# Optimization experiments

Hardware: AMD Instinct MI355X
Metric: run time of the kernel (lower is better)

## Reference

```python
import jax, jax.numpy as jnp
import numpy as np

# ---- config (mirrors init_kwargs) ----
T = 1024          # num tokens (one causal sequence)
H = 1024          # hidden_size
NQ, NK, D = 16, 4, 64   # q heads, kv heads, head_dim (GQA)
I_DENSE = 4096    # dense FFN intermediate
I_MOE = 512       # expert FFN intermediate
E, K = 8, 2       # num_experts, top_k
EPS = 1e-6
THETA = 10000.0


def setup_inputs() -> dict:
    key = jax.random.key(0)
    ks = jax.random.split(key, 20)
    rn = lambda k, shp: (jax.random.normal(k, shp, dtype=jnp.float32) * 0.02)
    QKV = (NQ + 2 * NK) * D
    return {
        "hidden_states": jax.random.normal(ks[0], (T, H), dtype=jnp.float32),
        "residual": jax.random.normal(ks[1], (T, H), dtype=jnp.float32),
        "positions": jnp.arange(T, dtype=jnp.int32),
        "ln0_w": jnp.ones((H,), jnp.float32),
        "pa0_w": jnp.ones((H,), jnp.float32),
        "ln1_w": jnp.ones((H,), jnp.float32),
        "pa1_w": jnp.ones((H,), jnp.float32),
        # attention weights (stored [in, out] so x @ W)
        "qkv0_w": rn(ks[2], (H, QKV)),
        "o0_w": rn(ks[3], (NQ * D, H)),
        "qkv1_w": rn(ks[4], (H, QKV)),
        "o1_w": rn(ks[5], (NQ * D, H)),
        # dense MLPs (merged gate_up: first half gate, second half up)
        "gu0_w": rn(ks[6], (H, 2 * I_DENSE)),
        "dn0_w": rn(ks[7], (I_DENSE, H)),
        "gu1_w": rn(ks[8], (H, 2 * I_DENSE)),
        "dn1_w": rn(ks[9], (I_DENSE, H)),
        # MoE: router gate + per-expert SwiGLU weights
        "gate_w": rn(ks[10], (H, E)),
        "w13": rn(ks[11], (E, H, 2 * I_MOE)),
        "w2": rn(ks[12], (E, I_MOE, H)),
    }


def _rmsnorm(x, w):
    v = jnp.mean(jnp.square(x.astype(jnp.float32)), axis=-1, keepdims=True)
    return (x.astype(jnp.float32) * jax.lax.rsqrt(v + EPS)).astype(x.dtype) * w


def _add_rmsnorm(x, res, w):
    # sglang fused add + RMSNorm: residual <- x + residual; out <- rmsnorm(residual)
    res = x + res
    return _rmsnorm(res, w), res


def _rope(pos, x):
    # neox-style rotary over full head_dim; x: [T, n_heads, D]
    half = D // 2
    inv_freq = 1.0 / (THETA ** (jnp.arange(half, dtype=jnp.float32) / half))
    f = pos.astype(jnp.float32)[:, None] * inv_freq            # [T, half]
    cos, sin = jnp.cos(f)[:, None, :], jnp.sin(f)[:, None, :]  # [T, 1, half]
    x1, x2 = x[..., :half], x[..., half:]
    return jnp.concatenate([x1 * cos - x2 * sin, x2 * cos + x1 * sin], axis=-1)


def _attention(pos, x, qkv_w, o_w):
    qkv = x @ qkv_w
    q = qkv[:, : NQ * D].reshape(T, NQ, D)
    k = qkv[:, NQ * D : (NQ + NK) * D].reshape(T, NK, D)
    v = qkv[:, (NQ + NK) * D :].reshape(T, NK, D)
    q, k = _rope(pos, q), _rope(pos, k)
    g = NQ // NK
    qg = q.reshape(T, NK, g, D)
    scores = jnp.einsum("tkgd,skd->kgts", qg, k) * (D ** -0.5)  # [NK,g,T,T]
    causal = jnp.tril(jnp.ones((T, T), bool))
    scores = jnp.where(causal, scores, jnp.float32(-1e30))
    p = jax.nn.softmax(scores, axis=-1)
    o = jnp.einsum("kgts,skd->tkgd", p, v).reshape(T, NQ * D)
    return o @ o_w


def _dense_mlp(x, gu_w, dn_w):
    gu = x @ gu_w
    h = jax.nn.silu(gu[:, :I_DENSE]) * gu[:, I_DENSE:]  # SiluAndMul
    return h @ dn_w


def _moe(x, gate_w, w13, w2):
    # router in fp32 (router_dtype == 'float32'), softmax, top-k, no renormalize
    logits = x.astype(jnp.float32) @ gate_w.astype(jnp.float32)  # [T, E]
    probs = jax.nn.softmax(logits, axis=-1)
    topw, topi = jax.lax.top_k(probs, K)                         # [T, K]
    rows = jnp.arange(x.shape[0])[:, None]
    combine = jnp.zeros((x.shape[0], E), jnp.float32).at[rows, topi].set(topw)
    combine = combine.astype(x.dtype)
    out = jnp.zeros_like(x)
    for e in range(E):  # fixed small expert count: grouped-GEMM reference
        g = x @ w13[e]
        h = jax.nn.silu(g[:, :I_MOE]) * g[:, I_MOE:]
        out = out + combine[:, e : e + 1] * (h @ w2[e])
    return out


def reference(hidden_states, residual, positions, ln0_w, pa0_w, ln1_w, pa1_w,
              qkv0_w, o0_w, qkv1_w, o1_w, gu0_w, dn0_w, gu1_w, dn1_w,
              gate_w, w13, w2):
    h, r = _add_rmsnorm(hidden_states, residual, ln0_w)
    h = _attention(positions, h, qkv0_w, o0_w)
    h, r = _add_rmsnorm(h, r, pa0_w)
    shortcut = _moe(h, gate_w, w13, w2)      # MoE runs on the shortcut branch
    h = _dense_mlp(h, gu0_w, dn0_w)
    h, r = _add_rmsnorm(h, r, ln1_w)
    h = _attention(positions, h, qkv1_w, o1_w)
    h, r = _add_rmsnorm(h, r, pa1_w)
    h = _dense_mlp(h, gu1_w, dn1_w)
    h = h + shortcut                          # combine shortcut MoE output
    return h, r
```

## Files before the change

### kernel.cpp

```cpp
#include <hip/hip_runtime.h>
#include <math.h>

namespace {

constexpr int kT = 1024;
constexpr int kH = 1024;
constexpr int kNQ = 16;
constexpr int kNKV = 4;
constexpr int kD = 64;
constexpr int kQKV = (kNQ + 2 * kNKV) * kD;
constexpr int kIDense = 4096;
constexpr int kIMoe = 512;
constexpr int kE = 8;
constexpr float kEps = 1e-6f;

typedef __attribute__((ext_vector_type(8))) short short8;
typedef __attribute__((ext_vector_type(4))) float f32x4;

__device__ __forceinline__ ushort f2bf(float f) {
    union { float f; uint32_t u; } v; v.f = f;
    uint32_t r = (v.u + 0x7fffu + ((v.u >> 16) & 1u)) >> 16;
    return (ushort)r;
}
__device__ __forceinline__ void gload16(const void* g, void* l) {
    __builtin_amdgcn_global_load_lds(
        (const __attribute__((address_space(1))) void*)g,
        (__attribute__((address_space(3))) void*)l, 16, 0, 0);
}

__global__ __launch_bounds__(256) void add_rmsnorm_kernel(
    const float* __restrict__ x, const float* __restrict__ res,
    const float* __restrict__ w, float* __restrict__ h32,
    ushort* __restrict__ h16, float* __restrict__ r_out)
{
    __shared__ float red[4];
    const int t = blockIdx.x;
    const int i = threadIdx.x;
    const size_t base = (size_t)t * kH;
    float4 a = reinterpret_cast<const float4*>(x + base)[i];
    float4 b = reinterpret_cast<const float4*>(res + base)[i];
    float4 s = make_float4(a.x + b.x, a.y + b.y, a.z + b.z, a.w + b.w);
    reinterpret_cast<float4*>(r_out + base)[i] = s;
    float ss = s.x * s.x + s.y * s.y + s.z * s.z + s.w * s.w;
    #pragma unroll
    for (int off = 32; off > 0; off >>= 1) ss += __shfl_down(ss, off);
    if ((i & 63) == 0) red[i >> 6] = ss;
    __syncthreads();
    const float tot = red[0] + red[1] + red[2] + red[3];
    const float inv = rsqrtf(tot * (1.0f / kH) + kEps);
    float4 wv = reinterpret_cast<const float4*>(w)[i];
    float4 o = make_float4(s.x * inv * wv.x, s.y * inv * wv.y,
                           s.z * inv * wv.z, s.w * inv * wv.w);
    reinterpret_cast<float4*>(h32 + base)[i] = o;
    ushort4 u;
    u.x = f2bf(o.x); u.y = f2bf(o.y); u.z = f2bf(o.z); u.w = f2bf(o.w);
    reinterpret_cast<ushort4*>(h16 + base)[i] = u;
}

__global__ __launch_bounds__(256) void transpose_bf16_kernel(
    const float* __restrict__ W, ushort* __restrict__ WT,
    int R, int Cn, int ld_w, long w_z_stride, long wt_z_stride)
{
    __shared__ float tile[64 * 65];
    const int z = blockIdx.z;
    const float* Wz = W + (size_t)z * w_z_stride;
    ushort* WTz = WT + (size_t)z * wt_z_stride;
    const int r0 = blockIdx.y * 64;
    const int c0 = blockIdx.x * 64;
    const int tid = threadIdx.x;
    const int lr = tid >> 4;
    const int lc = (tid & 15) * 4;
    #pragma unroll
    for (int p = 0; p < 4; p++) {
        const int row = p * 16 + lr;
        float4 v = *reinterpret_cast<const float4*>(
            &Wz[(size_t)(r0 + row) * ld_w + c0 + lc]);
        tile[row * 65 + lc + 0] = v.x;
        tile[row * 65 + lc + 1] = v.y;
        tile[row * 65 + lc + 2] = v.z;
        tile[row * 65 + lc + 3] = v.w;
    }
    __syncthreads();
    const int ocl = tid >> 2;
    const int q = tid & 3;
    ushort u[16];
    #pragma unroll
    for (int e = 0; e < 16; e++)
        u[e] = f2bf(tile[(q * 16 + e) * 65 + ocl]);
    ushort* dst = &WTz[(size_t)(c0 + ocl) * R + r0 + q * 16];
    *reinterpret_cast<short8*>(dst) = *reinterpret_cast<short8*>(&u[0]);
    *reinterpret_cast<short8*>(dst + 8) = *reinterpret_cast<short8*>(&u[8]);
}

template <bool GATED>
__global__ __launch_bounds__(256) void mgemm_kernel(
    const ushort* __restrict__ A, const ushort* __restrict__ B,
    float* __restrict__ Cf, ushort* __restrict__ C16,
    const float* __restrict__ scale,
    int lda, int ldb, int ldc, int kc,
    int gate_off_rows, long b_z_stride, int c_z_col, int k_z_off,
    int scale_stride, int atomic_flag)
{
    __shared__ __align__(16) ushort As[64 * 64];
    __shared__ __align__(16) ushort Bs[64 * 64];
    __shared__ __align__(16) ushort Us[GATED ? 64 * 64 : 8];

    const int z = blockIdx.z;
    const int m0 = blockIdx.y * 64;
    const int n0 = blockIdx.x * 64;
    const int tid = threadIdx.x;
    const ushort* Bz = B + (size_t)z * b_z_stride;
    const int k0 = z * k_z_off;

    const int arow = tid >> 3;
    const int achk = tid & 7;

    const int lane = tid & 63;
    const int wave = tid >> 6;
    const int wr = (wave >> 1) * 32;
    const int wc = (wave & 1) * 32;
    const int lrow = lane & 15;
    const int lg = lane >> 4;

    f32x4 accg[2][2] = {};
    f32x4 accu[2][2] = {};

    for (int kk0 = 0; kk0 < kc; kk0 += 64) {
        const int kbase = k0 + kk0;
        #pragma unroll
        for (int c = 0; c < 2; c++) {
            const int row = c * 32 + arow;
            const int cs = (achk + (row & 7)) & 7;
            gload16(A + (size_t)(m0 + row) * lda + kbase + cs * 8,
                    (char*)As + c * 4096 + tid * 16);
            gload16(Bz + (size_t)(n0 + row) * ldb + kbase + cs * 8,
                    (char*)Bs + c * 4096 + tid * 16);
            if constexpr (GATED)
                gload16(Bz + (size_t)(gate_off_rows + n0 + row) * ldb + kbase + cs * 8,
                        (char*)Us + c * 4096 + tid * 16);
        }
        __syncthreads();

        short8 af[2][2], bfr[2][2];
        #pragma unroll
        for (int mf = 0; mf < 2; mf++)
            #pragma unroll
            for (int kk = 0; kk < 2; kk++) {
                const int r = wr + mf * 16 + lrow;
                const int sl = ((kk * 4 + lg) - (r & 7)) & 7;
                af[mf][kk] = *reinterpret_cast<const short8*>(
                    (const char*)As + r * 128 + sl * 16);
            }
        #pragma unroll
        for (int nf = 0; nf < 2; nf++)
            #pragma unroll
            for (int kk = 0; kk < 2; kk++) {
                const int n = wc + nf * 16 + lrow;
                const int sl = ((kk * 4 + lg) - (n & 7)) & 7;
                bfr[nf][kk] = *reinterpret_cast<const short8*>(
                    (const char*)Bs + n * 128 + sl * 16);
            }
        #pragma unroll
        for (int mf = 0; mf < 2; mf++)
            #pragma unroll
            for (int nf = 0; nf < 2; nf++)
                #pragma unroll
                for (int kk = 0; kk < 2; kk++)
                    accg[mf][nf] = __builtin_amdgcn_mfma_f32_16x16x32_bf16(
                        af[mf][kk], bfr[nf][kk], accg[mf][nf], 0, 0, 0);
        if constexpr (GATED) {
            short8 uf[2][2];
            #pragma unroll
            for (int nf = 0; nf < 2; nf++)
                #pragma unroll
                for (int kk = 0; kk < 2; kk++) {
                    const int n = wc + nf * 16 + lrow;
                    const int sl = ((kk * 4 + lg) - (n & 7)) & 7;
                    uf[nf][kk] = *reinterpret_cast<const short8*>(
                        (const char*)Us + n * 128 + sl * 16);
                }
            #pragma unroll
            for (int mf = 0; mf < 2; mf++)
                #pragma unroll
                for (int nf = 0; nf < 2; nf++)
                    #pragma unroll
                    for (int kk = 0; kk < 2; kk++)
                        accu[mf][nf] = __builtin_amdgcn_mfma_f32_16x16x32_bf16(
                            af[mf][kk], uf[nf][kk], accu[mf][nf], 0, 0, 0);
        }
        __syncthreads();
    }

    const int r4 = (lane >> 4) * 4;
    const int cl = lane & 15;
    const int ccol = z * c_z_col;
    #pragma unroll
    for (int mf = 0; mf < 2; mf++) {
        #pragma unroll
        for (int nf = 0; nf < 2; nf++) {
            #pragma unroll
            for (int j = 0; j < 4; j++) {
                const int row = m0 + wr + mf * 16 + r4 + j;
                const int col = ccol + n0 + wc + nf * 16 + cl;
                if constexpr (GATED) {
                    const float g = accg[mf][nf][j];
                    const float u = accu[mf][nf][j];
                    const float sv =
                        scale ? scale[(size_t)row * scale_stride + z] : 1.0f;
                    const float h = (g / (1.0f + __expf(-g))) * u * sv;
                    C16[(size_t)row * ldc + col] = f2bf(h);
                } else if (atomic_flag) {
                    atomicAdd(&Cf[(size_t)row * ldc + col], accg[mf][nf][j]);
                } else {
                    Cf[(size_t)row * ldc + col] = accg[mf][nf][j];
                }
            }
        }
    }
}

__global__ __launch_bounds__(256) void rope_pack_kernel(
    const float* __restrict__ qkv, const int* __restrict__ positions,
    ushort* __restrict__ Qb, ushort* __restrict__ Kb)
{
    const int t = blockIdx.x;
    const float pos = (float)positions[t];
    for (int item = threadIdx.x; item < (kNQ + kNKV) * 32; item += 256) {
        const int head = item >> 5;
        const int i = item & 31;
        const float inv_freq = powf(10000.0f, -(float)i * (1.0f / 32.0f));
        const float f = pos * inv_freq;
        float sv, cv;
        sincosf(f, &sv, &cv);
        const size_t off = (size_t)t * kQKV + head * kD;
        const float x1 = qkv[off + i];
        const float x2 = qkv[off + 32 + i];
        const float r1 = x1 * cv - x2 * sv;
        const float r2 = x2 * cv + x1 * sv;
        if (head < kNQ) {
            ushort* q = Qb + ((size_t)head * kT + t) * kD;
            q[i] = f2bf(r1 * 0.125f);
            q[i + 32] = f2bf(r2 * 0.125f);
        } else {
            ushort* k = Kb + ((size_t)(head - kNQ) * kT + t) * kD;
            k[i] = f2bf(r1);
            k[i + 32] = f2bf(r2);
        }
    }
}

__global__ __launch_bounds__(64) void gate_topk_kernel(
    const float* __restrict__ h, const float* __restrict__ gate_w,
    float* __restrict__ combine)
{
    const int t = blockIdx.x;
    const int lane = threadIdx.x;
    float acc[kE] = {};
    for (int i = lane; i < kH; i += 64) {
        const float xv = h[(size_t)t * kH + i];
        const float* gw = gate_w + (size_t)i * kE;
        #pragma unroll
        for (int e = 0; e < kE; e++) acc[e] += xv * gw[e];
    }
    #pragma unroll
    for (int e = 0; e < kE; e++) {
        #pragma unroll
        for (int off = 32; off > 0; off >>= 1) acc[e] += __shfl_down(acc[e], off);
    }
    if (lane == 0) {
        float mx = acc[0];
        #pragma unroll
        for (int e = 1; e < kE; e++) mx = fmaxf(mx, acc[e]);
        float p[kE];
        float s = 0.0f;
        #pragma unroll
        for (int e = 0; e < kE; e++) { p[e] = expf(acc[e] - mx); s += p[e]; }
        const float invs = 1.0f / s;
        #pragma unroll
        for (int e = 0; e < kE; e++) p[e] *= invs;
        int i1 = 0;
        #pragma unroll
        for (int e = 1; e < kE; e++) if (p[e] > p[i1]) i1 = e;
        int i2 = (i1 == 0) ? 1 : 0;
        #pragma unroll
        for (int e = 0; e < kE; e++) if (e != i1 && p[e] > p[i2]) i2 = e;
        float outv[kE];
        #pragma unroll
        for (int e = 0; e < kE; e++) outv[e] = 0.0f;
        outv[i1] = p[i1];
        outv[i2] = p[i2];
        #pragma unroll
        for (int e = 0; e < kE; e++) combine[(size_t)t * kE + e] = outv[e];
    }
}

__global__ __launch_bounds__(256) void attn_mfma_kernel(
    const ushort* __restrict__ Qb, const ushort* __restrict__ Kb,
    const ushort* __restrict__ Vt, ushort* __restrict__ attn_o)
{
    __shared__ __align__(16) ushort Qs[64 * 64];
    __shared__ __align__(16) ushort Ks[64 * 64];
    __shared__ __align__(16) ushort Vs[64 * 64];
    __shared__ __align__(16) ushort Ps[64 * 64];
    const int tid = threadIdx.x;
    const int qb = blockIdx.x * 64;
    const int hq = blockIdx.y;
    const int kvh = hq >> 2;
    const int lane = tid & 63;
    const int wave = tid >> 6;
    const int lrow = lane & 15;
    const int g = lane >> 4;
    const int srow = tid >> 3;
    const int sx = tid & 7;
    const ushort* Qg = Qb + ((size_t)hq * kT + qb) * kD;
    const ushort* Kg = Kb + (size_t)kvh * kT * kD;
    const ushort* Vg = Vt + (size_t)kvh * kD * kT;
    const int xr = (lrow & 7) << 4;

    #pragma unroll
    for (int c = 0; c < 2; c++) {
        const int row = c * 32 + srow;
        gload16(Qg + (size_t)row * kD + ((sx ^ (row & 7)) * 8),
                (char*)Qs + c * 4096 + tid * 16);
    }
    __syncthreads();
    short8 qf[2];
    #pragma unroll
    for (int kk = 0; kk < 2; kk++)
        qf[kk] = *reinterpret_cast<const short8*>(
            (const char*)Qs + (16 * wave + lrow) * 128 + ((kk * 64 + g * 16) ^ xr));

    f32x4 oacc[4] = {};
    float mrow = -1e30f, lsum = 0.0f;

    for (int s0 = 0; s0 <= qb; s0 += 64) {
        __syncthreads();
        #pragma unroll
        for (int c = 0; c < 2; c++) {
            const int row = c * 32 + srow;
            gload16(Kg + (size_t)(s0 + row) * kD + ((sx ^ (row & 7)) * 8),
                    (char*)Ks + c * 4096 + tid * 16);
            gload16(Vg + (size_t)row * kT + s0 + ((sx ^ (row & 7)) * 8),
                    (char*)Vs + c * 4096 + tid * 16);
        }
        __syncthreads();

        f32x4 sacc[4] = {};
        #pragma unroll
        for (int nf = 0; nf < 4; nf++) {
            #pragma unroll
            for (int kk = 0; kk < 2; kk++) {
                short8 kf = *reinterpret_cast<const short8*>(
                    (const char*)Ks + (nf * 16 + lrow) * 128 + ((kk * 64 + g * 16) ^ xr));
                sacc[nf] = __builtin_amdgcn_mfma_f32_16x16x32_bf16(
                    kf, qf[kk], sacc[nf], 0, 0, 0);
            }
        }

        const bool diag = (s0 == qb);
        float pv[16];
        float mloc = -1e30f;
        #pragma unroll
        for (int nf = 0; nf < 4; nf++)
            #pragma unroll
            for (int j = 0; j < 4; j++) {
                float s = sacc[nf][j];
                if (diag && (nf * 16 + g * 4 + j > 16 * wave + lrow)) s = -1e30f;
                pv[nf * 4 + j] = s;
                mloc = fmaxf(mloc, s);
            }
        mloc = fmaxf(mloc, __shfl_xor(mloc, 16));
        mloc = fmaxf(mloc, __shfl_xor(mloc, 32));
        const float mnew = fmaxf(mrow, mloc);
        const float alpha = __expf(mrow - mnew);
        float psum = 0.0f;
        #pragma unroll
        for (int j = 0; j < 16; j++) { pv[j] = __expf(pv[j] - mnew); psum += pv[j]; }
        psum += __shfl_xor(psum, 16);
        psum += __shfl_xor(psum, 32);
        lsum = lsum * alpha + psum;
        mrow = mnew;

        const int prow = 16 * wave + lrow;
        #pragma unroll
        for (int nf = 0; nf < 4; nf++)
            #pragma unroll
            for (int jp = 0; jp < 2; jp++) {
                uint32_t pk = (uint32_t)f2bf(pv[nf * 4 + jp * 2]) |
                              ((uint32_t)f2bf(pv[nf * 4 + jp * 2 + 1]) << 16);
                *reinterpret_cast<uint32_t*>(
                    (char*)Ps + prow * 128 + ((nf * 32 + g * 8 + jp * 4) ^ xr)) = pk;
            }

        float aj[4];
        #pragma unroll
        for (int j = 0; j < 4; j++) aj[j] = __shfl(alpha, g * 4 + j);
        #pragma unroll
        for (int nf = 0; nf < 4; nf++)
            #pragma unroll
            for (int j = 0; j < 4; j++) oacc[nf][j] *= aj[j];

        short8 paf[2];
        #pragma unroll
        for (int kk = 0; kk < 2; kk++)
            paf[kk] = *reinterpret_cast<const short8*>(
                (const char*)Ps + prow * 128 + ((kk * 64 + g * 16) ^ xr));
        #pragma unroll
        for (int nf = 0; nf < 4; nf++)
            #pragma unroll
            for (int kk = 0; kk < 2; kk++) {
                short8 vf = *reinterpret_cast<const short8*>(
                    (const char*)Vs + (nf * 16 + lrow) * 128 + ((kk * 64 + g * 16) ^ xr));
                oacc[nf] = __builtin_amdgcn_mfma_f32_16x16x32_bf16(
                    paf[kk], vf, oacc[nf], 0, 0, 0);
            }
    }

    float lj[4];
    #pragma unroll
    for (int j = 0; j < 4; j++) lj[j] = 1.0f / __shfl(lsum, g * 4 + j);
    #pragma unroll
    for (int nf = 0; nf < 4; nf++)
        #pragma unroll
        for (int j = 0; j < 4; j++) {
            const int trow = qb + 16 * wave + g * 4 + j;
            attn_o[(size_t)trow * (kNQ * kD) + hq * kD + nf * 16 + lrow] =
                f2bf(oacc[nf][j] * lj[j]);
        }
}

__global__ __launch_bounds__(256) void final_out_kernel(
    const float* __restrict__ mlp, const float* __restrict__ shortcut,
    const float* __restrict__ r, float* __restrict__ out)
{
    const int i = blockIdx.x * 256 + threadIdx.x;
    float4 a = reinterpret_cast<const float4*>(mlp)[i];
    float4 b = reinterpret_cast<const float4*>(shortcut)[i];
    reinterpret_cast<float4*>(out)[i] =
        make_float4(a.x + b.x, a.y + b.y, a.z + b.z, a.w + b.w);
    reinterpret_cast<float4*>(out + (size_t)kT * kH)[i] =
        reinterpret_cast<const float4*>(r)[i];
}

}

extern "C" void kernel_launch(void* const* d_in, const int* in_sizes, int n_in,
                              void* d_out, int out_size, void* d_ws, size_t ws_size,
                              hipStream_t stream) {
    (void)in_sizes; (void)n_in; (void)out_size; (void)ws_size;
    const float* hidden   = (const float*)d_in[0];
    const float* residual = (const float*)d_in[1];
    const int*   positions= (const int*)d_in[2];
    const float* ln0_w    = (const float*)d_in[3];
    const float* pa0_w    = (const float*)d_in[4];
    const float* ln1_w    = (const float*)d_in[5];
    const float* pa1_w    = (const float*)d_in[6];
    const float* qkv0_w   = (const float*)d_in[7];
    const float* o0_w     = (const float*)d_in[8];
    const float* qkv1_w   = (const float*)d_in[9];
    const float* o1_w     = (const float*)d_in[10];
    const float* gu0_w    = (const float*)d_in[11];
    const float* dn0_w    = (const float*)d_in[12];
    const float* gu1_w    = (const float*)d_in[13];
    const float* dn1_w    = (const float*)d_in[14];
    const float* gate_w   = (const float*)d_in[15];
    const float* w13      = (const float*)d_in[16];
    const float* w2       = (const float*)d_in[17];
    float* out_h = (float*)d_out;

    char* wsb = (char*)d_ws;
    float*  r_buf   = (float*)(wsb + (0ull  << 20));
    float*  h32     = (float*)(wsb + (4ull  << 20));
    float*  t0_buf  = (float*)(wsb + (8ull  << 20));
    float*  qkv_buf = (float*)(wsb + (12ull << 20));
    float*  sc_buf  = (float*)(wsb + (18ull << 20));
    float*  cb_buf  = (float*)(wsb + (22ull << 20));
    ushort* h16     = (ushort*)(wsb + (23ull << 20));
    ushort* ao16    = (ushort*)(wsb + (25ull << 20));
    ushort* he16    = (ushort*)(wsb + (27ull << 20));
    ushort* wT      = (ushort*)(wsb + (35ull << 20));
    ushort* Qb      = (ushort*)(wsb + (40ull << 20));
    ushort* Kb      = (ushort*)(wsb + (42ull << 20));
    ushort* VtG     = (ushort*)(wsb + (43ull << 20));

    auto transp = [&](const float* W, int R, int Cn, int nz, long zs) {
        transpose_bf16_kernel<<<dim3(Cn / 64, R / 64, nz), 256, 0, stream>>>(
            W, wT, R, Cn, Cn, zs, zs);
    };
    auto gemm_f32 = [&](const ushort* A, float* C, int N, int lda_,
                        int ldb_, int ldc_, int nz, int kc, int kzoff, int atomic) {
        mgemm_kernel<false><<<dim3(N / 64, kT / 64, nz), 256, 0, stream>>>(
            A, wT, C, nullptr, nullptr, lda_, ldb_, ldc_, kc,
            0, 0, 0, kzoff, 0, atomic);
    };
    auto attention = [&](const float* qkv_w, const float* o_w) {
        transp(qkv_w, kH, kQKV, 1, 0);
        gemm_f32(h16, qkv_buf, kQKV, kH, kH, kQKV, 1, kH, 0, 0);
        rope_pack_kernel<<<kT, 256, 0, stream>>>(qkv_buf, positions, Qb, Kb);
        transpose_bf16_kernel<<<dim3(1, kT / 64, kNKV), 256, 0, stream>>>(
            qkv_buf + (kNQ + kNKV) * kD, VtG, kT, kD, kQKV, kD, (long)kD * kT);
        attn_mfma_kernel<<<dim3(kT / 64, kNQ), 256, 0, stream>>>(Qb, Kb, VtG, ao16);
        transp(o_w, kNQ * kD, kH, 1, 0);
        hipMemsetAsync(t0_buf, 0, (size_t)kT * kH * 4, stream);
        gemm_f32(ao16, t0_buf, kH, kNQ * kD, kNQ * kD, kH, 2, 512, 512, 1);
    };
    auto dense_mlp = [&](const float* gu_w, const float* dn_w) {
        transp(gu_w, kH, 2 * kIDense, 1, 0);
        mgemm_kernel<true><<<dim3(kIDense / 64, kT / 64, 1), 256, 0, stream>>>(
            h16, wT, nullptr, he16, nullptr, kH, kH, kIDense, kH,
            kIDense, 0, 0, 0, 0, 0);
        transp(dn_w, kIDense, kH, 1, 0);
        hipMemsetAsync(t0_buf, 0, (size_t)kT * kH * 4, stream);
        gemm_f32(he16, t0_buf, kH, kIDense, kIDense, kH, 4, 1024, 1024, 1);
    };

    add_rmsnorm_kernel<<<kT, 256, 0, stream>>>(hidden, residual, ln0_w, h32, h16, r_buf);
    attention(qkv0_w, o0_w);
    add_rmsnorm_kernel<<<kT, 256, 0, stream>>>(t0_buf, r_buf, pa0_w, h32, h16, r_buf);
    gate_topk_kernel<<<kT, 64, 0, stream>>>(h32, gate_w, cb_buf);
    transp(w13, kH, 2 * kIMoe, kE, (long)kH * 2 * kIMoe);
    mgemm_kernel<true><<<dim3(kIMoe / 64, kT / 64, kE), 256, 0, stream>>>(
        h16, wT, nullptr, he16, cb_buf, kH, kH, kIDense, kH,
        kIMoe, (long)kH * 2 * kIMoe, kIMoe, 0, kE, 0);
    transp(w2, kE * kIMoe, kH, 1, 0);
    hipMemsetAsync(sc_buf, 0, (size_t)kT * kH * 4, stream);
    gemm_f32(he16, sc_buf, kH, kIDense, kIDense, kH, 4, 1024, 1024, 1);
    dense_mlp(gu0_w, dn0_w);
    add_rmsnorm_kernel<<<kT, 256, 0, stream>>>(t0_buf, r_buf, ln1_w, h32, h16, r_buf);
    attention(qkv1_w, o1_w);
    add_rmsnorm_kernel<<<kT, 256, 0, stream>>>(t0_buf, r_buf, pa1_w, h32, h16, r_buf);
    dense_mlp(gu1_w, dn1_w);
    final_out_kernel<<<(kT * kH / 4) / 256, 256, 0, stream>>>(t0_buf, sc_buf, r_buf, out_h);
}
```

Before: 375.0 us.

## Route MoE tokens to experts and compute only selected token-expert pairs

The gate kernel now builds per-expert token counts and index lists with atomics. Two new grouped GEMM kernels gather only the routed tokens for each expert, for w13 with SwiGLU and for w2 with a scatter via atomicAdd. Previously all 8 experts were computed densely over all tokens. This is meant to cut MoE FLOPs by about a factor of four, at the cost of gather loads, early-exit blocks and nondeterministic token ordering from the atomics.

New measurement: 388.3 us. 1.04x slower.

```diff
diff --git a/kernel.cpp b/kernel.cpp
--- a/kernel.cpp
+++ b/kernel.cpp
@@ -213,6 +213,205 @@
                     atomicAdd(&Cf[(size_t)row * ldc + col], accg[mf][nf][j]);
                 } else {
                     Cf[(size_t)row * ldc + col] = accg[mf][nf][j];
+                }
+            }
+        }
+    }
+}
+
+__global__ __launch_bounds__(256) void moe_w13_kernel(
+    const ushort* __restrict__ Ah, const ushort* __restrict__ w13T,
+    ushort* __restrict__ heC, const float* __restrict__ combine,
+    const int* __restrict__ counts, const int* __restrict__ idx)
+{
+    const int e = blockIdx.z;
+    const int cnt = counts[e];
+    const int m0 = blockIdx.y * 64;
+    if (m0 >= cnt) return;
+    const int n0 = blockIdx.x * 64;
+
+    __shared__ __align__(16) ushort As[64 * 64];
+    __shared__ __align__(16) ushort Bs[64 * 64];
+    __shared__ __align__(16) ushort Us[64 * 64];
+
+    const ushort* Bz = w13T + (size_t)e * (2 * kIMoe) * kH;
+    const int* idxe = idx + e * kT;
+    const int tid = threadIdx.x;
+    const int arow = tid >> 3;
+    const int achk = tid & 7;
+    const int lane = tid & 63;
+    const int wave = tid >> 6;
+    const int wr = (wave >> 1) * 32;
+    const int wc = (wave & 1) * 32;
+    const int lrow = lane & 15;
+    const int lg = lane >> 4;
+
+    int tokA[2];
+    #pragma unroll
+    for (int c = 0; c < 2; c++) {
+        int gl = m0 + c * 32 + arow;
+        tokA[c] = idxe[gl < cnt ? gl : cnt - 1];
+    }
+
+    f32x4 accg[2][2] = {};
+    f32x4 accu[2][2] = {};
+
+    for (int kk0 = 0; kk0 < kH; kk0 += 64) {
+        #pragma unroll
+        for (int c = 0; c < 2; c++) {
+            const int row = c * 32 + arow;
+            const int cs = (achk + (row & 7)) & 7;
+            gload16(Ah + (size_t)tokA[c] * kH + kk0 + cs * 8,
+                    (char*)As + c * 4096 + tid * 16);
+            gload16(Bz + (size_t)(n0 + row) * kH + kk0 + cs * 8,
+                    (char*)Bs + c * 4096 + tid * 16);
+            gload16(Bz + (size_t)(kIMoe + n0 + row) * kH + kk0 + cs * 8,
+                    (char*)Us + c * 4096 + tid * 16);
+        }
+        __syncthreads();
+
+        short8 af[2][2], bfr[2][2], uf[2][2];
+        #pragma unroll
+        for (int mf = 0; mf < 2; mf++)
+            #pragma unroll
+            for (int kk = 0; kk < 2; kk++) {
+                const int r = wr + mf * 16 + lrow;
+                const int sl = ((kk * 4 + lg) - (r & 7)) & 7;
+                af[mf][kk] = *reinterpret_cast<const short8*>(
+                    (const char*)As + r * 128 + sl * 16);
+            }
+        #pragma unroll
+        for (int nf = 0; nf < 2; nf++)
+            #pragma unroll
+            for (int kk = 0; kk < 2; kk++) {
+                const int n = wc + nf * 16 + lrow;
+                const int sl = ((kk * 4 + lg) - (n & 7)) & 7;
+                bfr[nf][kk] = *reinterpret_cast<const short8*>(
+                    (const char*)Bs + n * 128 + sl * 16);
+                uf[nf][kk] = *reinterpret_cast<const short8*>(
+                    (const char*)Us + n * 128 + sl * 16);
+            }
+        #pragma unroll
+        for (int mf = 0; mf < 2; mf++)
+            #pragma unroll
+            for (int nf = 0; nf < 2; nf++)
+                #pragma unroll
+                for (int kk = 0; kk < 2; kk++) {
+                    accg[mf][nf] = __builtin_amdgcn_mfma_f32_16x16x32_bf16(
+                        af[mf][kk], bfr[nf][kk], accg[mf][nf], 0, 0, 0);
+                    accu[mf][nf] = __builtin_amdgcn_mfma_f32_16x16x32_bf16(
+                        af[mf][kk], uf[nf][kk], accu[mf][nf], 0, 0, 0);
+                }
+        __syncthreads();
+    }
+
+    const int r4 = (lane >> 4) * 4;
+    const int cl = lane & 15;
+    #pragma unroll
+    for (int mf = 0; mf < 2; mf++) {
+        #pragma unroll
+        for (int nf = 0; nf < 2; nf++) {
+            #pragma unroll
+            for (int j = 0; j < 4; j++) {
+                const int gl = m0 + wr + mf * 16 + r4 + j;
+                if (gl < cnt) {
+                    const int token = idxe[gl];
+                    const float sv = combine[(size_t)token * kE + e];
+                    const float g = accg[mf][nf][j];
+                    const float u = accu[mf][nf][j];
+                    const float h = (g / (1.0f + __expf(-g))) * u * sv;
+                    heC[((size_t)e * kT + gl) * kIMoe + n0 + wc + nf * 16 + cl] =
+                        f2bf(h);
+                }
+            }
+        }
+    }
+}
+
+__global__ __launch_bounds__(256) void moe_w2_kernel(
+    const ushort* __restrict__ heC, const ushort* __restrict__ w2T,
+    float* __restrict__ sc, const int* __restrict__ counts,
+    const int* __restrict__ idx)
+{
+    const int e = blockIdx.z;
+    const int cnt = counts[e];
+    const int m0 = blockIdx.y * 64;
+    if (m0 >= cnt) return;
+    const int n0 = blockIdx.x * 64;
+
+    __shared__ __align__(16) ushort As[64 * 64];
+    __shared__ __align__(16) ushort Bs[64 * 64];
+
+    const ushort* Az = heC + (size_t)e * kT * kIMoe;
+    const ushort* Bz = w2T + (size_t)e * kH * kIMoe;
+    const int* idxe = idx + e * kT;
+    const int tid = threadIdx.x;
+    const int arow = tid >> 3;
+    const int achk = tid & 7;
+    const int lane = tid & 63;
+    const int wave = tid >> 6;
+    const int wr = (wave >> 1) * 32;
+    const int wc = (wave & 1) * 32;
+    const int lrow = lane & 15;
+    const int lg = lane >> 4;
+
+    f32x4 acc[2][2] = {};
+
+    for (int kk0 = 0; kk0 < kIMoe; kk0 += 64) {
+        #pragma unroll
+        for (int c = 0; c < 2; c++) {
+            const int row = c * 32 + arow;
+            const int cs = (achk + (row & 7)) & 7;
+            gload16(Az + (size_t)(m0 + row) * kIMoe + kk0 + cs * 8,
+                    (char*)As + c * 4096 + tid * 16);
+            gload16(Bz + (size_t)(n0 + row) * kIMoe + kk0 + cs * 8,
+                    (char*)Bs + c * 4096 + tid * 16);
+        }
+        __syncthreads();
+
+        short8 af[2][2], bfr[2][2];
+        #pragma unroll
+        for (int mf = 0; mf < 2; mf++)
+            #pragma unroll
+            for (int kk = 0; kk < 2; kk++) {
+                const int r = wr + mf * 16 + lrow;
+                const int sl = ((kk * 4 + lg) - (r & 7)) & 7;
+                af[mf][kk] = *reinterpret_cast<const short8*>(
+                    (const char*)As + r * 128 + sl * 16);
+            }
+        #pragma unroll
+        for (int nf = 0; nf < 2; nf++)
+            #pragma unroll
+            for (int kk = 0; kk < 2; kk++) {
+                const int n = wc + nf * 16 + lrow;
+                const int sl = ((kk * 4 + lg) - (n & 7)) & 7;
+                bfr[nf][kk] = *reinterpret_cast<const short8*>(
+                    (const char*)Bs + n * 128 + sl * 16);
+            }
+        #pragma unroll
+        for (int mf = 0; mf < 2; mf++)
+            #pragma unroll
+            for (int nf = 0; nf < 2; nf++)
+                #pragma unroll
+                for (int kk = 0; kk < 2; kk++)
+                    acc[mf][nf] = __builtin_amdgcn_mfma_f32_16x16x32_bf16(
+                        af[mf][kk], bfr[nf][kk], acc[mf][nf], 0, 0, 0);
+        __syncthreads();
+    }
+
+    const int r4 = (lane >> 4) * 4;
+    const int cl = lane & 15;
+    #pragma unroll
+    for (int mf = 0; mf < 2; mf++) {
+        #pragma unroll
+        for (int nf = 0; nf < 2; nf++) {
+            #pragma unroll
+            for (int j = 0; j < 4; j++) {
+                const int gl = m0 + wr + mf * 16 + r4 + j;
+                if (gl < cnt) {
+                    const int token = idxe[gl];
+                    atomicAdd(&sc[(size_t)token * kH + n0 + wc + nf * 16 + cl],
+                              acc[mf][nf][j]);
                 }
             }
         }
@@ -251,7 +450,7 @@
 
 __global__ __launch_bounds__(64) void gate_topk_kernel(
     const float* __restrict__ h, const float* __restrict__ gate_w,
-    float* __restrict__ combine)
+    float* __restrict__ combine, int* __restrict__ counts, int* __restrict__ idx)
 {
     const int t = blockIdx.x;
     const int lane = threadIdx.x;
@@ -291,6 +490,10 @@
         outv[i2] = p[i2];
         #pragma unroll
         for (int e = 0; e < kE; e++) combine[(size_t)t * kE + e] = outv[e];
+        const int s1 = atomicAdd(&counts[i1], 1);
+        idx[i1 * kT + s1] = t;
+        const int s2 = atomicAdd(&counts[i2], 1);
+        idx[i2 * kT + s2] = t;
     }
 }
 
@@ -475,17 +678,19 @@
     float*  qkv_buf = (float*)(wsb + (12ull << 20));
     float*  sc_buf  = (float*)(wsb + (18ull << 20));
     float*  cb_buf  = (float*)(wsb + (22ull << 20));
+    int*    cnt_buf = (int*)  (wsb + (22ull << 20) + (1 << 15));
+    int*    idx_buf = (int*)  (wsb + (22ull << 20) + (1 << 16));
     ushort* h16     = (ushort*)(wsb + (23ull << 20));
     ushort* ao16    = (ushort*)(wsb + (25ull << 20));
-    ushort* he16    = (ushort*)(wsb + (27ull << 20));
+    ushort* heC     = (ushort*)(wsb + (27ull << 20));
     ushort* wT      = (ushort*)(wsb + (35ull << 20));
     ushort* Qb      = (ushort*)(wsb + (40ull << 20));
     ushort* Kb      = (ushort*)(wsb + (42ull << 20));
     ushort* VtG     = (ushort*)(wsb + (43ull << 20));
 
-    auto transp = [&](const float* W, int R, int Cn, int nz, long zs) {
+    auto transp = [&](const float* W, int R, int Cn, int nz, long zs_in, long zs_out) {
         transpose_bf16_kernel<<<dim3(Cn / 64, R / 64, nz), 256, 0, stream>>>(
-            W, wT, R, Cn, Cn, zs, zs);
+            W, wT, R, Cn, Cn, zs_in, zs_out);
     };
     auto gemm_f32 = [&](const ushort* A, float* C, int N, int lda_,
                         int ldb_, int ldc_, int nz, int kc, int kzoff, int atomic) {
@@ -494,37 +699,39 @@
             0, 0, 0, kzoff, 0, atomic);
     };
     auto attention = [&](const float* qkv_w, const float* o_w) {
-        transp(qkv_w, kH, kQKV, 1, 0);
+        transp(qkv_w, kH, kQKV, 1, 0, 0);
         gemm_f32(h16, qkv_buf, kQKV, kH, kH, kQKV, 1, kH, 0, 0);
         rope_pack_kernel<<<kT, 256, 0, stream>>>(qkv_buf, positions, Qb, Kb);
         transpose_bf16_kernel<<<dim3(1, kT / 64, kNKV), 256, 0, stream>>>(
             qkv_buf + (kNQ + kNKV) * kD, VtG, kT, kD, kQKV, kD, (long)kD * kT);
         attn_mfma_kernel<<<dim3(kT / 64, kNQ), 256, 0, stream>>>(Qb, Kb, VtG, ao16);
-        transp(o_w, kNQ * kD, kH, 1, 0);
+        transp(o_w, kNQ * kD, kH, 1, 0, 0);
         hipMemsetAsync(t0_buf, 0, (size_t)kT * kH * 4, stream);
         gemm_f32(ao16, t0_buf, kH, kNQ * kD, kNQ * kD, kH, 2, 512, 512, 1);
     };
     auto dense_mlp = [&](const float* gu_w, const float* dn_w) {
-        transp(gu_w, kH, 2 * kIDense, 1, 0);
+        transp(gu_w, kH, 2 * kIDense, 1, 0, 0);
         mgemm_kernel<true><<<dim3(kIDense / 64, kT / 64, 1), 256, 0, stream>>>(
-            h16, wT, nullptr, he16, nullptr, kH, kH, kIDense, kH,
+            h16, wT, nullptr, (ushort*)heC, nullptr, kH, kH, kIDense, kH,
             kIDense, 0, 0, 0, 0, 0);
-        transp(dn_w, kIDense, kH, 1, 0);
+        transp(dn_w, kIDense, kH, 1, 0, 0);
         hipMemsetAsync(t0_buf, 0, (size_t)kT * kH * 4, stream);
-        gemm_f32(he16, t0_buf, kH, kIDense, kIDense, kH, 4, 1024, 1024, 1);
+        gemm_f32((ushort*)heC, t0_buf, kH, kIDense, kIDense, kH, 4, 1024, 1024, 1);
     };
 
     add_rmsnorm_kernel<<<kT, 256, 0, stream>>>(hidden, residual, ln0_w, h32, h16, r_buf);
     attention(qkv0_w, o0_w);
     add_rmsnorm_kernel<<<kT, 256, 0, stream>>>(t0_buf, r_buf, pa0_w, h32, h16, r_buf);
-    gate_topk_kernel<<<kT, 64, 0, stream>>>(h32, gate_w, cb_buf);
-    transp(w13, kH, 2 * kIMoe, kE, (long)kH * 2 * kIMoe);
-    mgemm_kernel<true><<<dim3(kIMoe / 64, kT / 64, kE), 256, 0, stream>>>(
-        h16, wT, nullptr, he16, cb_buf, kH, kH, kIDense, kH,
-        kIMoe, (long)kH * 2 * kIMoe, kIMoe, 0, kE, 0);
-    transp(w2, kE * kIMoe, kH, 1, 0);
+    hipMemsetAsync(cnt_buf, 0, kE * sizeof(int), stream);
+    gate_topk_kernel<<<kT, 64, 0, stream>>>(h32, gate_w, cb_buf, cnt_buf, idx_buf);
+    transp(w13, kH, 2 * kIMoe, kE, (long)kH * 2 * kIMoe, (long)kH * 2 * kIMoe);
+    moe_w13_kernel<<<dim3(kIMoe / 64, kT / 64, kE), 256, 0, stream>>>(
+        h16, wT, heC, cb_buf, cnt_buf, idx_buf);
+    transpose_bf16_kernel<<<dim3(kH / 64, kIMoe / 64, kE), 256, 0, stream>>>(
+        w2, wT, kIMoe, kH, kH, (long)kIMoe * kH, (long)kH * kIMoe);
     hipMemsetAsync(sc_buf, 0, (size_t)kT * kH * 4, stream);
-    gemm_f32(he16, sc_buf, kH, kIDense, kIDense, kH, 4, 1024, 1024, 1);
+    moe_w2_kernel<<<dim3(kH / 64, kT / 64, kE), 256, 0, stream>>>(
+        heC, wT, sc_buf, cnt_buf, idx_buf);
     dense_mlp(gu0_w, dn0_w);
     add_rmsnorm_kernel<<<kT, 256, 0, stream>>>(t0_buf, r_buf, ln1_w, h32, h16, r_buf);
     attention(qkv1_w, o1_w);
```

## Replace split-K atomics with per-split partial buffers and add block-index swizzle

Applied to the files above, without the earlier changes.

Split-K GEMMs now write each K-slice to its own fp32 partial buffer instead of atomically adding into a zeroed output, and the downstream add_rmsnorm and final kernels sum the partials. This removes the hipMemsetAsync calls and the contention and serialization of atomics, at the cost of more workspace and extra reads in the reduction kernels. The GEMM also remaps its flat block ID so that consecutive blocks are spread in groups of eight, meant to improve L2 reuse of weight tiles. The workspace layout is reshuffled, with aliasing of cb_buf with t0P and of qkv_buf with he16.

Result: faster. 345.0 us (-8.0%).

```diff
diff --git a/kernel.cpp b/kernel.cpp
--- a/kernel.cpp
+++ b/kernel.cpp
@@ -13,6 +13,7 @@
 constexpr int kIMoe = 512;
 constexpr int kE = 8;
 constexpr float kEps = 1e-6f;
+constexpr long kTH = (long)kT * kH;
 
 typedef __attribute__((ext_vector_type(8))) short short8;
 typedef __attribute__((ext_vector_type(4))) float f32x4;
@@ -29,7 +30,7 @@
 }
 
 __global__ __launch_bounds__(256) void add_rmsnorm_kernel(
-    const float* __restrict__ x, const float* __restrict__ res,
+    const float* __restrict__ xP, int nparts, const float* __restrict__ res,
     const float* __restrict__ w, float* __restrict__ h32,
     ushort* __restrict__ h16, float* __restrict__ r_out)
 {
@@ -37,9 +38,11 @@
     const int t = blockIdx.x;
     const int i = threadIdx.x;
     const size_t base = (size_t)t * kH;
-    float4 a = reinterpret_cast<const float4*>(x + base)[i];
-    float4 b = reinterpret_cast<const float4*>(res + base)[i];
-    float4 s = make_float4(a.x + b.x, a.y + b.y, a.z + b.z, a.w + b.w);
+    float4 s = reinterpret_cast<const float4*>(res + base)[i];
+    for (int p = 0; p < nparts; p++) {
+        float4 a = reinterpret_cast<const float4*>(xP + p * kTH + base)[i];
+        s.x += a.x; s.y += a.y; s.z += a.z; s.w += a.w;
+    }
     reinterpret_cast<float4*>(r_out + base)[i] = s;
     float ss = s.x * s.x + s.y * s.y + s.z * s.z + s.w * s.w;
     #pragma unroll
@@ -99,15 +102,21 @@
     const float* __restrict__ scale,
     int lda, int ldb, int ldc, int kc,
     int gate_off_rows, long b_z_stride, int c_z_col, int k_z_off,
-    int scale_stride, int atomic_flag)
+    int scale_stride, long c_fstride)
 {
     __shared__ __align__(16) ushort As[64 * 64];
     __shared__ __align__(16) ushort Bs[64 * 64];
     __shared__ __align__(16) ushort Us[GATED ? 64 * 64 : 8];
 
     const int z = blockIdx.z;
-    const int m0 = blockIdx.y * 64;
-    const int n0 = blockIdx.x * 64;
+    const int gy = gridDim.y;
+    const int nf = gridDim.x * gy;
+    const int fid = blockIdx.x + gridDim.x * blockIdx.y;
+    const int qq = nf >> 3;
+    const int id2 = (fid & 7) * qq + (fid >> 3);
+    const int m0 = (id2 % gy) * 64;
+    const int n0 = (id2 / gy) * 64;
+
     const int tid = threadIdx.x;
     const ushort* Bz = B + (size_t)z * b_z_stride;
     const int k0 = z * k_z_off;
@@ -152,41 +161,41 @@
                     (const char*)As + r * 128 + sl * 16);
             }
         #pragma unroll
-        for (int nf = 0; nf < 2; nf++)
+        for (int nf2 = 0; nf2 < 2; nf2++)
             #pragma unroll
             for (int kk = 0; kk < 2; kk++) {
-                const int n = wc + nf * 16 + lrow;
+                const int n = wc + nf2 * 16 + lrow;
                 const int sl = ((kk * 4 + lg) - (n & 7)) & 7;
-                bfr[nf][kk] = *reinterpret_cast<const short8*>(
+                bfr[nf2][kk] = *reinterpret_cast<const short8*>(
                     (const char*)Bs + n * 128 + sl * 16);
             }
         #pragma unroll
         for (int mf = 0; mf < 2; mf++)
             #pragma unroll
-            for (int nf = 0; nf < 2; nf++)
+            for (int nf2 = 0; nf2 < 2; nf2++)
                 #pragma unroll
                 for (int kk = 0; kk < 2; kk++)
-                    accg[mf][nf] = __builtin_amdgcn_mfma_f32_16x16x32_bf16(
-                        af[mf][kk], bfr[nf][kk], accg[mf][nf], 0, 0, 0);
+                    accg[mf][nf2] = __builtin_amdgcn_mfma_f32_16x16x32_bf16(
+                        af[mf][kk], bfr[nf2][kk], accg[mf][nf2], 0, 0, 0);
         if constexpr (GATED) {
             short8 uf[2][2];
             #pragma unroll
-            for (int nf = 0; nf < 2; nf++)
+            for (int nf2 = 0; nf2 < 2; nf2++)
                 #pragma unroll
                 for (int kk = 0; kk < 2; kk++) {
-                    const int n = wc + nf * 16 + lrow;
+                    const int n = wc + nf2 * 16 + lrow;
                     const int sl = ((kk * 4 + lg) - (n & 7)) & 7;
-                    uf[nf][kk] = *reinterpret_cast<const short8*>(
+                    uf[nf2][kk] = *reinterpret_cast<const short8*>(
                         (const char*)Us + n * 128 + sl * 16);
                 }
             #pragma unroll
             for (int mf = 0; mf < 2; mf++)
                 #pragma unroll
-                for (int nf = 0; nf < 2; nf++)
+                for (int nf2 = 0; nf2 < 2; nf2++)
                     #pragma unroll
                     for (int kk = 0; kk < 2; kk++)
-                        accu[mf][nf] = __builtin_amdgcn_mfma_f32_16x16x32_bf16(
-                            af[mf][kk], uf[nf][kk], accu[mf][nf], 0, 0, 0);
+                        accu[mf][nf2] = __builtin_amdgcn_mfma_f32_16x16x32_bf16(
+                            af[mf][kk], uf[nf2][kk], accu[mf][nf2], 0, 0, 0);
         }
         __syncthreads();
     }
@@ -194,25 +203,24 @@
     const int r4 = (lane >> 4) * 4;
     const int cl = lane & 15;
     const int ccol = z * c_z_col;
+    float* Cfz = Cf ? Cf + (size_t)z * c_fstride : nullptr;
     #pragma unroll
     for (int mf = 0; mf < 2; mf++) {
         #pragma unroll
-        for (int nf = 0; nf < 2; nf++) {
+        for (int nf2 = 0; nf2 < 2; nf2++) {
             #pragma unroll
             for (int j = 0; j < 4; j++) {
                 const int row = m0 + wr + mf * 16 + r4 + j;
-                const int col = ccol + n0 + wc + nf * 16 + cl;
+                const int col = ccol + n0 + wc + nf2 * 16 + cl;
                 if constexpr (GATED) {
-                    const float g = accg[mf][nf][j];
-                    const float u = accu[mf][nf][j];
+                    const float g = accg[mf][nf2][j];
+                    const float u = accu[mf][nf2][j];
                     const float sv =
                         scale ? scale[(size_t)row * scale_stride + z] : 1.0f;
                     const float h = (g / (1.0f + __expf(-g))) * u * sv;
                     C16[(size_t)row * ldc + col] = f2bf(h);
-                } else if (atomic_flag) {
-                    atomicAdd(&Cf[(size_t)row * ldc + col], accg[mf][nf][j]);
                 } else {
-                    Cf[(size_t)row * ldc + col] = accg[mf][nf][j];
+                    Cfz[(size_t)row * ldc + col] = accg[mf][nf2][j];
                 }
             }
         }
@@ -430,15 +438,19 @@
 }
 
 __global__ __launch_bounds__(256) void final_out_kernel(
-    const float* __restrict__ mlp, const float* __restrict__ shortcut,
+    const float* __restrict__ mlpP, const float* __restrict__ scP,
     const float* __restrict__ r, float* __restrict__ out)
 {
     const int i = blockIdx.x * 256 + threadIdx.x;
-    float4 a = reinterpret_cast<const float4*>(mlp)[i];
-    float4 b = reinterpret_cast<const float4*>(shortcut)[i];
-    reinterpret_cast<float4*>(out)[i] =
-        make_float4(a.x + b.x, a.y + b.y, a.z + b.z, a.w + b.w);
-    reinterpret_cast<float4*>(out + (size_t)kT * kH)[i] =
+    float4 s = make_float4(0.f, 0.f, 0.f, 0.f);
+    #pragma unroll
+    for (int p = 0; p < 4; p++) {
+        float4 a = reinterpret_cast<const float4*>(mlpP + p * kTH)[i];
+        float4 b = reinterpret_cast<const float4*>(scP + p * kTH)[i];
+        s.x += a.x + b.x; s.y += a.y + b.y; s.z += a.z + b.z; s.w += a.w + b.w;
+    }
+    reinterpret_cast<float4*>(out)[i] = s;
+    reinterpret_cast<float4*>(out + kTH)[i] =
         reinterpret_cast<const float4*>(r)[i];
 }
 
@@ -471,64 +483,63 @@
     char* wsb = (char*)d_ws;
     float*  r_buf   = (float*)(wsb + (0ull  << 20));
     float*  h32     = (float*)(wsb + (4ull  << 20));
-    float*  t0_buf  = (float*)(wsb + (8ull  << 20));
-    float*  qkv_buf = (float*)(wsb + (12ull << 20));
-    float*  sc_buf  = (float*)(wsb + (18ull << 20));
-    float*  cb_buf  = (float*)(wsb + (22ull << 20));
-    ushort* h16     = (ushort*)(wsb + (23ull << 20));
-    ushort* ao16    = (ushort*)(wsb + (25ull << 20));
-    ushort* he16    = (ushort*)(wsb + (27ull << 20));
-    ushort* wT      = (ushort*)(wsb + (35ull << 20));
-    ushort* Qb      = (ushort*)(wsb + (40ull << 20));
-    ushort* Kb      = (ushort*)(wsb + (42ull << 20));
-    ushort* VtG     = (ushort*)(wsb + (43ull << 20));
-
-    auto transp = [&](const float* W, int R, int Cn, int nz, long zs) {
+    float*  t0P     = (float*)(wsb + (8ull  << 20));
+    float*  cb_buf  = (float*)(wsb + (8ull  << 20));
+    float*  scP     = (float*)(wsb + (24ull << 20));
+    ushort* h16     = (ushort*)(wsb + (40ull << 20));
+    ushort* ao16    = (ushort*)(wsb + (42ull << 20));
+    float*  qkv_buf = (float*)(wsb + (44ull << 20));
+    ushort* he16    = (ushort*)(wsb + (44ull << 20));
+    ushort* wT      = (ushort*)(wsb + (52ull << 20));
+    ushort* Qb      = (ushort*)(wsb + (62ull << 20));
+    ushort* Kb      = (ushort*)(wsb + (64ull << 20));
+    ushort* VtG     = (ushort*)(wsb + (65ull << 20));
+
+    auto transp = [&](const float* W, int R, int Cn, int nz, long zs_in, long zs_out) {
         transpose_bf16_kernel<<<dim3(Cn / 64, R / 64, nz), 256, 0, stream>>>(
-            W, wT, R, Cn, Cn, zs, zs);
+            W, wT, R, Cn, Cn, zs_in, zs_out);
     };
     auto gemm_f32 = [&](const ushort* A, float* C, int N, int lda_,
-                        int ldb_, int ldc_, int nz, int kc, int kzoff, int atomic) {
+                        int ldb_, int ldc_, int nz, int kc, int kzoff) {
         mgemm_kernel<false><<<dim3(N / 64, kT / 64, nz), 256, 0, stream>>>(
             A, wT, C, nullptr, nullptr, lda_, ldb_, ldc_, kc,
-            0, 0, 0, kzoff, 0, atomic);
+            0, 0, 0, kzoff, 0, kTH);
     };
     auto attention = [&](const float* qkv_w, const float* o_w) {
-        transp(qkv_w, kH, kQKV, 1, 0);
-        gemm_f32(h16, qkv_buf, kQKV, kH, kH, kQKV, 1, kH, 0, 0);
+        transp(qkv_w, kH, kQKV, 1, 0, 0);
+        mgemm_kernel<false><<<dim3(kQKV / 64, kT / 64, 1), 256, 0, stream>>>(
+            h16, wT, qkv_buf, nullptr, nullptr, kH, kH, kQKV, kH,
+            0, 0, 0, 0, 0, 0);
         rope_pack_kernel<<<kT, 256, 0, stream>>>(qkv_buf, positions, Qb, Kb);
         transpose_bf16_kernel<<<dim3(1, kT / 64, kNKV), 256, 0, stream>>>(
             qkv_buf + (kNQ + kNKV) * kD, VtG, kT, kD, kQKV, kD, (long)kD * kT);
         attn_mfma_kernel<<<dim3(kT / 64, kNQ), 256, 0, stream>>>(Qb, Kb, VtG, ao16);
-        transp(o_w, kNQ * kD, kH, 1, 0);
-        hipMemsetAsync(t0_buf, 0, (size_t)kT * kH * 4, stream);
-        gemm_f32(ao16, t0_buf, kH, kNQ * kD, kNQ * kD, kH, 2, 512, 512, 1);
+        transp(o_w, kNQ * kD, kH, 1, 0, 0);
+        gemm_f32(ao16, t0P, kH, kNQ * kD, kNQ * kD, kH, 2, 512, 512);
     };
     auto dense_mlp = [&](const float* gu_w, const float* dn_w) {
-        transp(gu_w, kH, 2 * kIDense, 1, 0);
+        transp(gu_w, kH, 2 * kIDense, 1, 0, 0);
         mgemm_kernel<true><<<dim3(kIDense / 64, kT / 64, 1), 256, 0, stream>>>(
             h16, wT, nullptr, he16, nullptr, kH, kH, kIDense, kH,
             kIDense, 0, 0, 0, 0, 0);
-        transp(dn_w, kIDense, kH, 1, 0);
-        hipMemsetAsync(t0_buf, 0, (size_t)kT * kH * 4, stream);
-        gemm_f32(he16, t0_buf, kH, kIDense, kIDense, kH, 4, 1024, 1024, 1);
+        transp(dn_w, kIDense, kH, 1, 0, 0);
+        gemm_f32(he16, t0P, kH, kIDense, kIDense, kH, 4, 1024, 1024);
     };
 
-    add_rmsnorm_kernel<<<kT, 256, 0, stream>>>(hidden, residual, ln0_w, h32, h16, r_buf);
+    add_rmsnorm_kernel<<<kT, 256, 0, stream>>>(hidden, 1, residual, ln0_w, h32, h16, r_buf);
     attention(qkv0_w, o0_w);
-    add_rmsnorm_kernel<<<kT, 256, 0, stream>>>(t0_buf, r_buf, pa0_w, h32, h16, r_buf);
+    add_rmsnorm_kernel<<<kT, 256, 0, stream>>>(t0P, 2, r_buf, pa0_w, h32, h16, r_buf);
     gate_topk_kernel<<<kT, 64, 0, stream>>>(h32, gate_w, cb_buf);
-    transp(w13, kH, 2 * kIMoe, kE, (long)kH * 2 * kIMoe);
+    transp(w13, kH, 2 * kIMoe, kE, (long)kH * 2 * kIMoe, (long)kH * 2 * kIMoe);
     mgemm_kernel<true><<<dim3(kIMoe / 64, kT / 64, kE), 256, 0, stream>>>(
         h16, wT, nullptr, he16, cb_buf, kH, kH, kIDense, kH,
         kIMoe, (long)kH * 2 * kIMoe, kIMoe, 0, kE, 0);
-    transp(w2, kE * kIMoe, kH, 1, 0);
-    hipMemsetAsync(sc_buf, 0, (size_t)kT * kH * 4, stream);
-    gemm_f32(he16, sc_buf, kH, kIDense, kIDense, kH, 4, 1024, 1024, 1);
+    transp(w2, kE * kIMoe, kH, 1, 0, 0);
+    gemm_f32(he16, scP, kH, kIDense, kIDense, kH, 4, 1024, 1024);
     dense_mlp(gu0_w, dn0_w);
-    add_rmsnorm_kernel<<<kT, 256, 0, stream>>>(t0_buf, r_buf, ln1_w, h32, h16, r_buf);
+    add_rmsnorm_kernel<<<kT, 256, 0, stream>>>(t0P, 4, r_buf, ln1_w, h32, h16, r_buf);
     attention(qkv1_w, o1_w);
-    add_rmsnorm_kernel<<<kT, 256, 0, stream>>>(t0_buf, r_buf, pa1_w, h32, h16, r_buf);
+    add_rmsnorm_kernel<<<kT, 256, 0, stream>>>(t0P, 2, r_buf, pa1_w, h32, h16, r_buf);
     dense_mlp(gu1_w, dn1_w);
-    final_out_kernel<<<(kT * kH / 4) / 256, 256, 0, stream>>>(t0_buf, sc_buf, r_buf, out_h);
-}
+    final_out_kernel<<<(kT * kH / 4) / 256, 256, 0, stream>>>(t0P, scP, r_buf, out_h);
+}
```
